# Performance work log

Hardware: AMD Instinct MI355X
Metric: run time of the kernel (lower is better)

Reference implementation:

```python
import jax, jax.numpy as jnp
import numpy as np

NUM_CLASS = 31
B = 4096
F_IN = 2048
F_BOT = 256


def setup_inputs() -> dict:
    key = jax.random.key(0)
    ks = jax.random.split(key, 6)
    return {
        "source": jax.random.normal(ks[0], (B, F_IN), dtype=jnp.float32),
        "target": jax.random.normal(ks[1], (B, F_IN), dtype=jnp.float32),
        "W_b": jax.random.normal(ks[2], (F_IN, F_BOT), dtype=jnp.float32) * (1.0 / np.sqrt(F_IN)),
        "b_b": jnp.zeros((F_BOT,), dtype=jnp.float32),
        "W_c": jax.random.normal(ks[3], (F_BOT, NUM_CLASS), dtype=jnp.float32) * (1.0 / np.sqrt(F_BOT)),
        "b_c": jnp.zeros((NUM_CLASS,), dtype=jnp.float32),
        "source_label": jax.random.randint(ks[4], (B,), 0, NUM_CLASS, dtype=jnp.int64),
    }


def _conf_margin(logits, labels):
    # get_confidence_output_margin: softmax confidence margin vs best wrong class
    conf = jax.nn.softmax(logits, axis=-1)
    mask = jax.nn.one_hot(labels, NUM_CLASS, dtype=conf.dtype)
    targets_conf = jnp.sum(conf * mask, axis=1)
    max_excl_conf = jnp.max(conf * (1.0 - mask), axis=1)
    return targets_conf - max_excl_conf


def _pairwise_sqdist(s, t):
    # ||x_p - x_q||^2 computed as a single GEMM + broadcast (replaces python double loop)
    s2 = jnp.sum(s * s, axis=1)  # [Bs]
    t2 = jnp.sum(t * t, axis=1)  # [Bt]
    d2 = s2[:, None] + t2[None, :] - 2.0 * (s @ t.T)
    return jnp.maximum(d2, 0.0)


def reference(source, target, W_b, b_b, W_c, b_c, source_label):
    # bottleneck: Linear + ReLU (shared weights for both domains)
    src = jax.nn.relu(source @ W_b + b_b)  # [B, 256]
    tar = jax.nn.relu(target @ W_b + b_b)  # [B, 256]

    src_clf = src @ W_c + b_c  # [B, 31]
    tar_clf = tar @ W_c + b_c  # [B, 31]

    # cross entropy on source
    logp = jax.nn.log_softmax(src_clf, axis=-1)
    clf_loss = -jnp.mean(jnp.take_along_axis(logp, source_label[:, None], axis=1))

    src_margin = _conf_margin(src_clf, source_label)
    tar_margin = _conf_margin(tar_clf, jnp.argmax(tar_clf, axis=1))

    # no_grad diagnostics: MMD + Gaussian kernel means (amplitude=1, sigma in {1,5})
    delta = jnp.mean(src, axis=0) - jnp.mean(tar, axis=0)
    curr_mmd = jax.lax.stop_gradient(delta @ delta)
    d2 = _pairwise_sqdist(src, tar)  # [B, B]
    curr_gk1 = jax.lax.stop_gradient(jnp.mean(jnp.exp(-0.5 * d2)))
    curr_gk5 = jax.lax.stop_gradient(jnp.mean(jnp.exp(-d2 / 50.0)))

    return jnp.concatenate([
        jnp.stack([clf_loss, curr_mmd, curr_gk1, curr_gk5]),
        src_margin,
        tar_margin,
    ])  # [4 + 2B]
```

## Files before the change

kernel.cpp:

```cpp
#include <hip/hip_runtime.h>
#include <stdint.h>

#define DI __device__ __forceinline__

typedef float f32x4 __attribute__((ext_vector_type(4)));
typedef short bf16x8 __attribute__((ext_vector_type(8)));

DI uint16_t f2bf(float f) {
    union { float f; uint32_t u; } v; v.f = f;
    uint32_t r = v.u + 0x7FFF + ((v.u >> 16) & 1);
    return (uint16_t)(r >> 16);
}
DI float bf2f(uint16_t h) {
    union { uint32_t u; float f; } v; v.u = ((uint32_t)h) << 16;
    return v.f;
}
DI void gl_lds16(const void* g, void* l) {
    __builtin_amdgcn_global_load_lds(
        (__attribute__((address_space(1))) void*)(uintptr_t)g,
        (__attribute__((address_space(3))) void*)(uintptr_t)l,
        16, 0, 0);
}

__global__ void k_init(const float* __restrict__ Wc, uint16_t* __restrict__ WcT,
                       float* __restrict__ accs) {
    int tid = threadIdx.x;
    if (tid < 4) accs[tid] = 0.f;
    for (int idx = tid; idx < 32 * 256; idx += 256) {
        int n = idx >> 8, k = idx & 255;
        WcT[idx] = (n < 31) ? f2bf(Wc[k * 31 + n]) : (uint16_t)0;
    }
}

__global__ void k_transpose_wb(const float* __restrict__ Wb, uint16_t* __restrict__ WbT) {
    __shared__ float t[32][33];
    int kb = blockIdx.x, nb = blockIdx.y;
    int tx = threadIdx.x & 31, ty0 = (threadIdx.x >> 5) * 4;
    for (int i = 0; i < 4; ++i)
        t[ty0 + i][tx] = Wb[(kb * 32 + ty0 + i) * 256 + nb * 32 + tx];
    __syncthreads();
    for (int i = 0; i < 4; ++i)
        WbT[(nb * 32 + ty0 + i) * 2048 + kb * 32 + tx] = f2bf(t[tx][ty0 + i]);
}

__launch_bounds__(256)
__global__ void k_bottleneck(const float* __restrict__ src, const float* __restrict__ tgt,
                             const uint16_t* __restrict__ WbT, const float* __restrict__ bb,
                             uint16_t* __restrict__ Y) {
    __shared__ __align__(16) uint8_t lds[20480];
    int tid = threadIdx.x;
    int lane = tid & 63, w = tid >> 6;
    int bm = blockIdx.x >> 1, bn = blockIdx.x & 1;
    int m0 = bm * 32;
    const float* X = (m0 < 4096) ? (src + (size_t)m0 * 2048)
                                 : (tgt + (size_t)(m0 - 4096) * 2048);
    int ar = tid >> 3, akb = (tid >> 2) & 1, ap = tid & 3;
    int ac = ap ^ (ar & 3) ^ ((ar >> 2) & 3);
    const float* Ag = X + ar * 2048 + akb * 32 + ac * 8;
    uint8_t* Aw = lds + akb * 2048 + ar * 64 + ap * 16;
    int cc = (lane >> 4) ^ (lane & 3) ^ ((lane >> 2) & 3);
    f32x4 acc[2][2] = {};
    for (int t = 0; t < 32; ++t) {
        int k0 = t * 64;
        if (t) __syncthreads();
        for (int i = 0; i < 4; ++i) {
            int s = w * 4 + i;
            int kb = s >> 3, r0 = (s & 7) * 16;
            int r = r0 + (lane >> 2), p = lane & 3;
            int c = p ^ (r & 3) ^ ((r >> 2) & 3);
            gl_lds16(WbT + (size_t)(bn * 128 + r) * 2048 + k0 + kb * 32 + c * 8,
                     lds + 4096 + s * 1024);
        }
        float4 x0 = *(const float4*)(Ag + k0);
        float4 x1 = *(const float4*)(Ag + k0 + 4);
        uint4 u;
        u.x = (uint32_t)f2bf(x0.x) | ((uint32_t)f2bf(x0.y) << 16);
        u.y = (uint32_t)f2bf(x0.z) | ((uint32_t)f2bf(x0.w) << 16);
        u.z = (uint32_t)f2bf(x1.x) | ((uint32_t)f2bf(x1.y) << 16);
        u.w = (uint32_t)f2bf(x1.z) | ((uint32_t)f2bf(x1.w) << 16);
        *(uint4*)Aw = u;
        __syncthreads();
        for (int kb = 0; kb < 2; ++kb) {
            bf16x8 a[2], b[2];
            for (int mi = 0; mi < 2; ++mi) {
                int r = mi * 16 + (lane & 15);
                a[mi] = *(const bf16x8*)(lds + kb * 2048 + r * 64 + cc * 16);
            }
            for (int nf = 0; nf < 2; ++nf) {
                int rn = w * 32 + nf * 16 + (lane & 15);
                b[nf] = *(const bf16x8*)(lds + 4096 + kb * 8192 + rn * 64 + cc * 16);
            }
            for (int mi = 0; mi < 2; ++mi)
                for (int nf = 0; nf < 2; ++nf)
                    acc[mi][nf] = __builtin_amdgcn_mfma_f32_16x16x32_bf16(
                        a[mi], b[nf], acc[mi][nf], 0, 0, 0);
        }
    }
    for (int mi = 0; mi < 2; ++mi)
        for (int nf = 0; nf < 2; ++nf) {
            int col = bn * 128 + w * 32 + nf * 16 + (lane & 15);
            float bias = bb[col];
            for (int j = 0; j < 4; ++j) {
                int row = m0 + mi * 16 + (lane >> 4) * 4 + j;
                float v = acc[mi][nf][j] + bias;
                v = fmaxf(v, 0.f);
                Y[(size_t)row * 256 + col] = f2bf(v);
            }
        }
}

__launch_bounds__(256)
__global__ void k_stats(const uint16_t* __restrict__ Y, float* __restrict__ s2t2,
                        float* __restrict__ colsum_part) {
    __shared__ float cs[4][256];
    int tid = threadIdx.x, lane = tid & 63, w = tid >> 6;
    int r0 = blockIdx.x * 32 + w * 8;
    float c0 = 0.f, c1 = 0.f, c2 = 0.f, c3 = 0.f;
    for (int i = 0; i < 8; ++i) {
        int row = r0 + i;
        ushort4 v = *(const ushort4*)(Y + (size_t)row * 256 + lane * 4);
        float a = bf2f(v.x), b = bf2f(v.y), c = bf2f(v.z), d = bf2f(v.w);
        c0 += a; c1 += b; c2 += c; c3 += d;
        float s = a * a + b * b + c * c + d * d;
        for (int m = 1; m < 64; m <<= 1) s += __shfl_xor(s, m);
        if (lane == 0) s2t2[row] = s;
    }
    cs[w][lane * 4 + 0] = c0;
    cs[w][lane * 4 + 1] = c1;
    cs[w][lane * 4 + 2] = c2;
    cs[w][lane * 4 + 3] = c3;
    __syncthreads();
    colsum_part[blockIdx.x * 256 + tid] =
        cs[0][tid] + cs[1][tid] + cs[2][tid] + cs[3][tid];
}

__launch_bounds__(256)
__global__ void k_classifier(const uint16_t* __restrict__ Y, const uint16_t* __restrict__ WcT,
                             const float* __restrict__ bc, const int* __restrict__ labels,
                             float* __restrict__ out_margin, float* __restrict__ ce_acc) {
    __shared__ __align__(16) uint8_t lds[49152];
    int tid = threadIdx.x, lane = tid & 63, w = tid >> 6;
    int m0 = blockIdx.x * 64;
    int cc = (lane >> 4) ^ (lane & 3) ^ ((lane >> 2) & 3);
    for (int s = w; s < 48; s += 4) {
        int r, p, c;
        if (s < 32) {
            int kb = s >> 2, r0 = (s & 3) * 16;
            r = r0 + (lane >> 2); p = lane & 3;
            c = p ^ (r & 3) ^ ((r >> 2) & 3);
            gl_lds16(Y + (size_t)(m0 + r) * 256 + kb * 32 + c * 8, lds + s * 1024);
        } else {
            int s2 = s - 32;
            int kb = s2 >> 1, r0 = (s2 & 1) * 16;
            r = r0 + (lane >> 2); p = lane & 3;
            c = p ^ (r & 3) ^ ((r >> 2) & 3);
            gl_lds16(WcT + r * 256 + kb * 32 + c * 8, lds + 32768 + s2 * 1024);
        }
    }
    __syncthreads();
    f32x4 acc[2] = {};
    for (int kb = 0; kb < 8; ++kb) {
        int r = w * 16 + (lane & 15);
        bf16x8 a = *(const bf16x8*)(lds + kb * 4096 + r * 64 + cc * 16);
        for (int nf = 0; nf < 2; ++nf) {
            int rn = nf * 16 + (lane & 15);
            bf16x8 b = *(const bf16x8*)(lds + 32768 + kb * 2048 + rn * 64 + cc * 16);
            acc[nf] = __builtin_amdgcn_mfma_f32_16x16x32_bf16(a, b, acc[nf], 0, 0, 0);
        }
    }
    int c0 = lane & 15, c1 = 16 + c0;
    float bc0 = bc[c0];
    float bc1 = (c1 < 31) ? bc[c1] : 0.f;
    bool is_src = (m0 < 4096);
    float ce_local = 0.f;
    for (int j = 0; j < 4; ++j) {
        int row = m0 + w * 16 + (lane >> 4) * 4 + j;
        float v0 = acc[0][j] + bc0;
        float v1 = (c1 < 31) ? (acc[1][j] + bc1) : -1e30f;
        float mx = fmaxf(v0, v1);
        for (int m = 1; m < 16; m <<= 1) mx = fmaxf(mx, __shfl_xor(mx, m, 16));
        float e0 = __expf(v0 - mx);
        float e1 = (c1 < 31) ? __expf(v1 - mx) : 0.f;
        float ssum = e0 + e1;
        for (int m = 1; m < 16; m <<= 1) ssum += __shfl_xor(ssum, m, 16);
        float inv = 1.f / ssum;
        float conf0 = e0 * inv, conf1 = e1 * inv;
        int lab;
        if (is_src) {
            lab = labels[row];
        } else {
            float bv; int bi;
            if (v0 >= v1) { bv = v0; bi = c0; } else { bv = v1; bi = c1; }
            for (int m = 1; m < 16; m <<= 1) {
                float ov = __shfl_xor(bv, m, 16);
                int oi = __shfl_xor(bi, m, 16);
                if (ov > bv || (ov == bv && oi < bi)) { bv = ov; bi = oi; }
            }
            lab = bi;
        }
        float tc = (c0 == lab ? conf0 : 0.f) + (c1 == lab ? conf1 : 0.f);
        for (int m = 1; m < 16; m <<= 1) tc += __shfl_xor(tc, m, 16);
        float ex = fmaxf(c0 == lab ? -1.f : conf0,
                         (c1 == lab || c1 >= 31) ? -1.f : conf1);
        for (int m = 1; m < 16; m <<= 1) ex = fmaxf(ex, __shfl_xor(ex, m, 16));
        if (c0 == 0) out_margin[row] = tc - ex;
        if (is_src) {
            float vl = (c0 == lab) ? v0 : ((c1 == lab) ? v1 : -1e30f);
            for (int m = 1; m < 16; m <<= 1) vl = fmaxf(vl, __shfl_xor(vl, m, 16));
            if (c0 == 0) ce_local += -(vl - mx - __logf(ssum));
        }
    }
    if (is_src) {
        ce_local += __shfl_xor(ce_local, 16);
        ce_local += __shfl_xor(ce_local, 32);
        if (lane == 0) atomicAdd(ce_acc, ce_local);
    }
}

__launch_bounds__(256)
__global__ void k_pairwise(const uint16_t* __restrict__ Y, const float* __restrict__ s2t2,
                           float* __restrict__ gk_part) {
    __shared__ __align__(16) uint8_t lds[65536];
    int tid = threadIdx.x, lane = tid & 63, w = tid >> 6;
    int m0 = blockIdx.x * 128, n0 = blockIdx.y * 128;
    int cc = (lane >> 4) ^ (lane & 3) ^ ((lane >> 2) & 3);
    int wm = (w & 1) * 64, wn = (w >> 1) * 64;
    f32x4 acc[4][4] = {};
    for (int h = 0; h < 2; ++h) {
        if (h) __syncthreads();
        int k0 = h * 128;
        for (int i = 0; i < 8; ++i) {
            int s = w * 8 + i;
            int kb = s >> 3, r0 = (s & 7) * 16;
            int r = r0 + (lane >> 2), p = lane & 3;
            int c = p ^ (r & 3) ^ ((r >> 2) & 3);
            gl_lds16(Y + (size_t)(m0 + r) * 256 + k0 + kb * 32 + c * 8, lds + s * 1024);
            gl_lds16(Y + (size_t)(4096 + n0 + r) * 256 + k0 + kb * 32 + c * 8,
                     lds + 32768 + s * 1024);
        }
        __syncthreads();
        for (int kb = 0; kb < 4; ++kb) {
            bf16x8 a[4], b[4];
            for (int mi = 0; mi < 4; ++mi) {
                int r = wm + mi * 16 + (lane & 15);
                a[mi] = *(const bf16x8*)(lds + kb * 8192 + r * 64 + cc * 16);
            }
            for (int nf = 0; nf < 4; ++nf) {
                int rn = wn + nf * 16 + (lane & 15);
                b[nf] = *(const bf16x8*)(lds + 32768 + kb * 8192 + rn * 64 + cc * 16);
            }
            for (int mi = 0; mi < 4; ++mi)
                for (int nf = 0; nf < 4; ++nf)
                    acc[mi][nf] = __builtin_amdgcn_mfma_f32_16x16x32_bf16(
                        a[mi], b[nf], acc[mi][nf], 0, 0, 0);
        }
    }
    float t2v[4];
    for (int nf = 0; nf < 4; ++nf)
        t2v[nf] = s2t2[4096 + n0 + wn + nf * 16 + (lane & 15)];
    float g1 = 0.f, g5 = 0.f;
    for (int mi = 0; mi < 4; ++mi) {
        int rbase = m0 + wm + mi * 16 + (lane >> 4) * 4;
        float s2v[4];
        for (int j = 0; j < 4; ++j) s2v[j] = s2t2[rbase + j];
        for (int nf = 0; nf < 4; ++nf)
            for (int j = 0; j < 4; ++j) {
                float d2 = s2v[j] + t2v[nf] - 2.f * acc[mi][nf][j];
                d2 = fmaxf(d2, 0.f);
                g1 += __expf(-0.5f * d2);
                g5 += __expf(-0.02f * d2);
            }
    }
    for (int m = 1; m < 64; m <<= 1) { g1 += __shfl_xor(g1, m); g5 += __shfl_xor(g5, m); }
    __syncthreads();
    float* red = (float*)lds;
    if (lane == 0) { red[w * 2] = g1; red[w * 2 + 1] = g5; }
    __syncthreads();
    if (tid == 0) {
        int bid = blockIdx.y * 32 + blockIdx.x;
        gk_part[bid * 2]     = red[0] + red[2] + red[4] + red[6];
        gk_part[bid * 2 + 1] = red[1] + red[3] + red[5] + red[7];
    }
}

__global__ void k_finalize(const float* __restrict__ colsum_part,
                           const float* __restrict__ gk_part,
                           const float* __restrict__ accs, float* __restrict__ d_out) {
    __shared__ float red[12];
    int tid = threadIdx.x, lane = tid & 63, w = tid >> 6;
    float cs = 0.f, ct = 0.f;
    for (int b = 0; b < 128; ++b)   cs += colsum_part[b * 256 + tid];
    for (int b = 128; b < 256; ++b) ct += colsum_part[b * 256 + tid];
    float delta = (cs - ct) * (1.f / 4096.f);
    float sq = delta * delta;
    float g1 = 0.f, g5 = 0.f;
    for (int i = 0; i < 4; ++i) {
        int p = tid * 4 + i;
        g1 += gk_part[p * 2];
        g5 += gk_part[p * 2 + 1];
    }
    for (int m = 1; m < 64; m <<= 1) {
        sq += __shfl_xor(sq, m);
        g1 += __shfl_xor(g1, m);
        g5 += __shfl_xor(g5, m);
    }
    if (lane == 0) { red[w * 3] = sq; red[w * 3 + 1] = g1; red[w * 3 + 2] = g5; }
    __syncthreads();
    if (tid == 0) {
        d_out[0] = accs[0] * (1.f / 4096.f);
        d_out[1] = red[0] + red[3] + red[6] + red[9];
        d_out[2] = (red[1] + red[4] + red[7] + red[10]) * 5.9604644775390625e-08f;
        d_out[3] = (red[2] + red[5] + red[8] + red[11]) * 5.9604644775390625e-08f;
    }
}

extern "C" void kernel_launch(void* const* d_in, const int* in_sizes, int n_in,
                              void* d_out, int out_size, void* d_ws, size_t ws_size,
                              hipStream_t stream) {
    const float* source = (const float*)d_in[0];
    const float* target = (const float*)d_in[1];
    const float* Wb     = (const float*)d_in[2];
    const float* bb     = (const float*)d_in[3];
    const float* Wc     = (const float*)d_in[4];
    const float* bc     = (const float*)d_in[5];
    const int*   labels = (const int*)d_in[6];
    float* out = (float*)d_out;
    uint8_t* ws = (uint8_t*)d_ws;

    uint16_t* Y    = (uint16_t*)(ws);
    uint16_t* WbT  = (uint16_t*)(ws + 4194304);
    uint16_t* WcT  = (uint16_t*)(ws + 5242880);
    float*    s2t2 = (float*)(ws + 5259264);
    float*    accs = (float*)(ws + 5292032);
    float*    colsum_part = (float*)(ws + 4194304);
    float*    gk_part     = (float*)(ws + 4194304 + 262144);

    k_init<<<1, 256, 0, stream>>>(Wc, WcT, accs);
    k_transpose_wb<<<dim3(64, 8), 256, 0, stream>>>(Wb, WbT);
    k_bottleneck<<<512, 256, 0, stream>>>(source, target, WbT, bb, Y);
    k_stats<<<256, 256, 0, stream>>>(Y, s2t2, colsum_part);
    k_classifier<<<128, 256, 0, stream>>>(Y, WcT, bc, labels, out + 4, accs);
    k_pairwise<<<dim3(32, 32), 256, 0, stream>>>(Y, s2t2, gk_part);
    k_finalize<<<1, 256, 0, stream>>>(colsum_part, gk_part, accs, out);
}
```

Measured before the change: 180.1 us.

## Double-buffer bottleneck GEMM LDS and prefetch next A/B tiles

Doubles the LDS allocation so the bottleneck GEMM keeps two stages of A and B tiles. The next tile's B is loaded into LDS and the next A rows are prefetched into registers while MFMAs run on the current stage. Explicit vmcnt/lgkmcnt waits plus a single barrier per stage replace the two syncthreads per iteration, which is meant to hide global memory latency behind compute. In exchange, the larger LDS footprint may lower occupancy, and the hand-written waitcnt counts are fragile.

```diff
diff --git a/kernel.cpp b/kernel.cpp
--- a/kernel.cpp
+++ b/kernel.cpp
@@ -47,7 +47,7 @@
 __global__ void k_bottleneck(const float* __restrict__ src, const float* __restrict__ tgt,
                              const uint16_t* __restrict__ WbT, const float* __restrict__ bb,
                              uint16_t* __restrict__ Y) {
-    __shared__ __align__(16) uint8_t lds[20480];
+    __shared__ __align__(16) uint8_t lds[40960];
     int tid = threadIdx.x;
     int lane = tid & 63, w = tid >> 6;
     int bm = blockIdx.x >> 1, bn = blockIdx.x & 1;
@@ -57,45 +57,117 @@
     int ar = tid >> 3, akb = (tid >> 2) & 1, ap = tid & 3;
     int ac = ap ^ (ar & 3) ^ ((ar >> 2) & 3);
     const float* Ag = X + ar * 2048 + akb * 32 + ac * 8;
-    uint8_t* Aw = lds + akb * 2048 + ar * 64 + ap * 16;
+    const int AwOff = akb * 2048 + ar * 64 + ap * 16;
     int cc = (lane >> 4) ^ (lane & 3) ^ ((lane >> 2) & 3);
+    const uint16_t* Bg0; const uint16_t* Bg1; const uint16_t* Bg2; const uint16_t* Bg3;
+    {
+        int p = lane & 3;
+        int i0 = w * 4;
+        #define BGADDR(ii) ({ int s_ = i0 + (ii); int kb_ = s_ >> 3; \
+            int r_ = (s_ & 7) * 16 + (lane >> 2); \
+            int c_ = p ^ (r_ & 3) ^ ((r_ >> 2) & 3); \
+            WbT + (size_t)(bn * 128 + r_) * 2048 + kb_ * 32 + c_ * 8; })
+        Bg0 = BGADDR(0); Bg1 = BGADDR(1); Bg2 = BGADDR(2); Bg3 = BGADDR(3);
+        #undef BGADDR
+    }
+    const int lbB = 8192 + w * 4096;
+
     f32x4 acc[2][2] = {};
-    for (int t = 0; t < 32; ++t) {
-        int k0 = t * 64;
-        if (t) __syncthreads();
-        for (int i = 0; i < 4; ++i) {
-            int s = w * 4 + i;
-            int kb = s >> 3, r0 = (s & 7) * 16;
-            int r = r0 + (lane >> 2), p = lane & 3;
-            int c = p ^ (r & 3) ^ ((r >> 2) & 3);
-            gl_lds16(WbT + (size_t)(bn * 128 + r) * 2048 + k0 + kb * 32 + c * 8,
-                     lds + 4096 + s * 1024);
-        }
-        float4 x0 = *(const float4*)(Ag + k0);
-        float4 x1 = *(const float4*)(Ag + k0 + 4);
-        uint4 u;
-        u.x = (uint32_t)f2bf(x0.x) | ((uint32_t)f2bf(x0.y) << 16);
-        u.y = (uint32_t)f2bf(x0.z) | ((uint32_t)f2bf(x0.w) << 16);
-        u.z = (uint32_t)f2bf(x1.x) | ((uint32_t)f2bf(x1.y) << 16);
-        u.w = (uint32_t)f2bf(x1.z) | ((uint32_t)f2bf(x1.w) << 16);
-        *(uint4*)Aw = u;
-        __syncthreads();
-        for (int kb = 0; kb < 2; ++kb) {
-            bf16x8 a[2], b[2];
-            for (int mi = 0; mi < 2; ++mi) {
-                int r = mi * 16 + (lane & 15);
-                a[mi] = *(const bf16x8*)(lds + kb * 2048 + r * 64 + cc * 16);
-            }
-            for (int nf = 0; nf < 2; ++nf) {
-                int rn = w * 32 + nf * 16 + (lane & 15);
-                b[nf] = *(const bf16x8*)(lds + 4096 + kb * 8192 + rn * 64 + cc * 16);
-            }
-            for (int mi = 0; mi < 2; ++mi)
-                for (int nf = 0; nf < 2; ++nf)
-                    acc[mi][nf] = __builtin_amdgcn_mfma_f32_16x16x32_bf16(
-                        a[mi], b[nf], acc[mi][nf], 0, 0, 0);
-        }
-    }
+    float4 rE0, rE1, rO0, rO1;
+
+    #define STAGE_B(par, k0) do { \
+        gl_lds16(Bg0 + (k0), lds + lbB + (par) * 16384 + 0);    \
+        gl_lds16(Bg1 + (k0), lds + lbB + (par) * 16384 + 1024); \
+        gl_lds16(Bg2 + (k0), lds + lbB + (par) * 16384 + 2048); \
+        gl_lds16(Bg3 + (k0), lds + lbB + (par) * 16384 + 3072); \
+    } while (0)
+
+    #define WRITE_A(par, r0v, r1v) do { \
+        uint4 u_; \
+        u_.x = (uint32_t)f2bf((r0v).x) | ((uint32_t)f2bf((r0v).y) << 16); \
+        u_.y = (uint32_t)f2bf((r0v).z) | ((uint32_t)f2bf((r0v).w) << 16); \
+        u_.z = (uint32_t)f2bf((r1v).x) | ((uint32_t)f2bf((r1v).y) << 16); \
+        u_.w = (uint32_t)f2bf((r1v).z) | ((uint32_t)f2bf((r1v).w) << 16); \
+        *(uint4*)(lds + (par) * 4096 + AwOff) = u_; \
+    } while (0)
+
+    #define COMPUTE(par) do { \
+        _Pragma("unroll") \
+        for (int kb = 0; kb < 2; ++kb) { \
+            bf16x8 a_[2], b_[2]; \
+            _Pragma("unroll") \
+            for (int mi = 0; mi < 2; ++mi) \
+                a_[mi] = *(const bf16x8*)(lds + (par) * 4096 + kb * 2048 + \
+                                          (mi * 16 + (lane & 15)) * 64 + cc * 16); \
+            _Pragma("unroll") \
+            for (int nf = 0; nf < 2; ++nf) \
+                b_[nf] = *(const bf16x8*)(lds + 8192 + (par) * 16384 + kb * 8192 + \
+                                          (w * 32 + nf * 16 + (lane & 15)) * 64 + cc * 16); \
+            _Pragma("unroll") \
+            for (int mi = 0; mi < 2; ++mi) \
+                _Pragma("unroll") \
+                for (int nf = 0; nf < 2; ++nf) \
+                    acc[mi][nf] = __builtin_amdgcn_mfma_f32_16x16x32_bf16( \
+                        a_[mi], b_[nf], acc[mi][nf], 0, 0, 0); \
+        } \
+    } while (0)
+
+    #define FENCE() asm volatile("" ::: "memory")
+
+    STAGE_B(0, 0);
+    FENCE();
+    rE0 = *(const float4*)(Ag);
+    rE1 = *(const float4*)(Ag + 4);
+    FENCE();
+    rO0 = *(const float4*)(Ag + 64);
+    rO1 = *(const float4*)(Ag + 68);
+    asm volatile("s_waitcnt vmcnt(2)" ::: "memory");
+    WRITE_A(0, rE0, rE1);
+    asm volatile("s_waitcnt lgkmcnt(0)" ::: "memory");
+    __builtin_amdgcn_s_barrier();
+
+    for (int tt = 0; tt < 15; ++tt) {
+        {
+            int t = 2 * tt;
+            STAGE_B(1, (t + 1) * 64);
+            FENCE();
+            rE0 = *(const float4*)(Ag + (t + 2) * 64);
+            rE1 = *(const float4*)(Ag + (t + 2) * 64 + 4);
+            FENCE();
+            COMPUTE(0);
+            asm volatile("s_waitcnt vmcnt(6)" ::: "memory");
+            WRITE_A(1, rO0, rO1);
+            asm volatile("s_waitcnt vmcnt(2) lgkmcnt(0)" ::: "memory");
+            __builtin_amdgcn_s_barrier();
+        }
+        {
+            int t = 2 * tt + 1;
+            STAGE_B(0, (t + 1) * 64);
+            FENCE();
+            rO0 = *(const float4*)(Ag + (t + 2) * 64);
+            rO1 = *(const float4*)(Ag + (t + 2) * 64 + 4);
+            FENCE();
+            COMPUTE(1);
+            asm volatile("s_waitcnt vmcnt(6)" ::: "memory");
+            WRITE_A(0, rE0, rE1);
+            asm volatile("s_waitcnt vmcnt(2) lgkmcnt(0)" ::: "memory");
+            __builtin_amdgcn_s_barrier();
+        }
+    }
+    STAGE_B(1, 31 * 64);
+    FENCE();
+    COMPUTE(0);
+    asm volatile("s_waitcnt vmcnt(4)" ::: "memory");
+    WRITE_A(1, rO0, rO1);
+    asm volatile("s_waitcnt vmcnt(0) lgkmcnt(0)" ::: "memory");
+    __builtin_amdgcn_s_barrier();
+    COMPUTE(1);
+
+    #undef STAGE_B
+    #undef WRITE_A
+    #undef COMPUTE
+    #undef FENCE
+
     for (int mi = 0; mi < 2; ++mi)
         for (int nf = 0; nf < 2; ++nf) {
             int col = bn * 128 + w * 32 + nf * 16 + (lane & 15);
```

New measurement: 174.6 us. -3.0%, faster.

## Restructure bottleneck GEMM as split-K across waves with LDS reduction

Applied to the files above, without the earlier changes.

The bottleneck GEMM now runs 256 blocks of 512 threads. Each block covers 32 rows and all 256 output columns, so every source/target row is read from global memory once instead of twice. Each of 8 waves handles a 256-wide K slice, loading A fragments directly from global into registers with double buffering and B fragments directly from global without LDS staging. Partial results are then reduced across waves through a 64KB LDS buffer before the bias and ReLU are applied. This removes the per-iteration syncthreads and the LDS staging, at the cost of 128 accumulator registers per thread, uncoalesced direct global B loads, and a reduction epilogue.

```diff
diff --git a/kernel.cpp b/kernel.cpp
--- a/kernel.cpp
+++ b/kernel.cpp
@@ -14,6 +14,14 @@
 DI float bf2f(uint16_t h) {
     union { uint32_t u; float f; } v; v.u = ((uint32_t)h) << 16;
     return v.f;
+}
+DI bf16x8 cvt8(float4 lo, float4 hi) {
+    union { uint4 u; bf16x8 v; } x;
+    x.u.x = (uint32_t)f2bf(lo.x) | ((uint32_t)f2bf(lo.y) << 16);
+    x.u.y = (uint32_t)f2bf(lo.z) | ((uint32_t)f2bf(lo.w) << 16);
+    x.u.z = (uint32_t)f2bf(hi.x) | ((uint32_t)f2bf(hi.y) << 16);
+    x.u.w = (uint32_t)f2bf(hi.z) | ((uint32_t)f2bf(hi.w) << 16);
+    return x.v;
 }
 DI void gl_lds16(const void* g, void* l) {
     __builtin_amdgcn_global_load_lds(
@@ -43,70 +51,83 @@
         WbT[(nb * 32 + ty0 + i) * 2048 + kb * 32 + tx] = f2bf(t[tx][ty0 + i]);
 }
 
-__launch_bounds__(256)
+__launch_bounds__(512, 2)
 __global__ void k_bottleneck(const float* __restrict__ src, const float* __restrict__ tgt,
                              const uint16_t* __restrict__ WbT, const float* __restrict__ bb,
                              uint16_t* __restrict__ Y) {
-    __shared__ __align__(16) uint8_t lds[20480];
-    int tid = threadIdx.x;
-    int lane = tid & 63, w = tid >> 6;
-    int bm = blockIdx.x >> 1, bn = blockIdx.x & 1;
-    int m0 = bm * 32;
+    __shared__ float red[8][2048];
+    int tid = threadIdx.x, lane = tid & 63, w = tid >> 6;
+    int m0 = blockIdx.x * 32;
     const float* X = (m0 < 4096) ? (src + (size_t)m0 * 2048)
                                  : (tgt + (size_t)(m0 - 4096) * 2048);
-    int ar = tid >> 3, akb = (tid >> 2) & 1, ap = tid & 3;
-    int ac = ap ^ (ar & 3) ^ ((ar >> 2) & 3);
-    const float* Ag = X + ar * 2048 + akb * 32 + ac * 8;
-    uint8_t* Aw = lds + akb * 2048 + ar * 64 + ap * 16;
-    int cc = (lane >> 4) ^ (lane & 3) ^ ((lane >> 2) & 3);
-    f32x4 acc[2][2] = {};
-    for (int t = 0; t < 32; ++t) {
-        int k0 = t * 64;
-        if (t) __syncthreads();
-        for (int i = 0; i < 4; ++i) {
-            int s = w * 4 + i;
-            int kb = s >> 3, r0 = (s & 7) * 16;
-            int r = r0 + (lane >> 2), p = lane & 3;
-            int c = p ^ (r & 3) ^ ((r >> 2) & 3);
-            gl_lds16(WbT + (size_t)(bn * 128 + r) * 2048 + k0 + kb * 32 + c * 8,
-                     lds + 4096 + s * 1024);
-        }
-        float4 x0 = *(const float4*)(Ag + k0);
-        float4 x1 = *(const float4*)(Ag + k0 + 4);
-        uint4 u;
-        u.x = (uint32_t)f2bf(x0.x) | ((uint32_t)f2bf(x0.y) << 16);
-        u.y = (uint32_t)f2bf(x0.z) | ((uint32_t)f2bf(x0.w) << 16);
-        u.z = (uint32_t)f2bf(x1.x) | ((uint32_t)f2bf(x1.y) << 16);
-        u.w = (uint32_t)f2bf(x1.z) | ((uint32_t)f2bf(x1.w) << 16);
-        *(uint4*)Aw = u;
-        __syncthreads();
-        for (int kb = 0; kb < 2; ++kb) {
-            bf16x8 a[2], b[2];
+    int fr = lane & 15;
+    int kq = lane >> 4;
+    const float* Ag = X + (size_t)fr * 2048 + w * 256 + kq * 8;
+    const uint16_t* Bg = WbT + (size_t)fr * 2048 + w * 256 + kq * 8;
+
+    f32x4 acc[2][16] = {};
+
+    float4 aA[2][2][2];
+    #pragma unroll
+    for (int mi = 0; mi < 2; ++mi) {
+        aA[0][mi][0] = *(const float4*)(Ag + mi * 32768);
+        aA[0][mi][1] = *(const float4*)(Ag + mi * 32768 + 4);
+        aA[1][mi][0] = *(const float4*)(Ag + mi * 32768 + 32);
+        aA[1][mi][1] = *(const float4*)(Ag + mi * 32768 + 36);
+    }
+    #pragma unroll
+    for (int t = 0; t < 8; ++t) {
+        bf16x8 af[2];
+        #pragma unroll
+        for (int mi = 0; mi < 2; ++mi)
+            af[mi] = cvt8(aA[t & 1][mi][0], aA[t & 1][mi][1]);
+        if (t < 6) {
+            #pragma unroll
             for (int mi = 0; mi < 2; ++mi) {
-                int r = mi * 16 + (lane & 15);
-                a[mi] = *(const bf16x8*)(lds + kb * 2048 + r * 64 + cc * 16);
-            }
-            for (int nf = 0; nf < 2; ++nf) {
-                int rn = w * 32 + nf * 16 + (lane & 15);
-                b[nf] = *(const bf16x8*)(lds + 4096 + kb * 8192 + rn * 64 + cc * 16);
-            }
-            for (int mi = 0; mi < 2; ++mi)
-                for (int nf = 0; nf < 2; ++nf)
-                    acc[mi][nf] = __builtin_amdgcn_mfma_f32_16x16x32_bf16(
-                        a[mi], b[nf], acc[mi][nf], 0, 0, 0);
-        }
-    }
-    for (int mi = 0; mi < 2; ++mi)
-        for (int nf = 0; nf < 2; ++nf) {
-            int col = bn * 128 + w * 32 + nf * 16 + (lane & 15);
-            float bias = bb[col];
-            for (int j = 0; j < 4; ++j) {
-                int row = m0 + mi * 16 + (lane >> 4) * 4 + j;
-                float v = acc[mi][nf][j] + bias;
-                v = fmaxf(v, 0.f);
-                Y[(size_t)row * 256 + col] = f2bf(v);
-            }
-        }
+                aA[t & 1][mi][0] = *(const float4*)(Ag + mi * 32768 + (t + 2) * 32);
+                aA[t & 1][mi][1] = *(const float4*)(Ag + mi * 32768 + (t + 2) * 32 + 4);
+            }
+        }
+        #pragma unroll
+        for (int nf = 0; nf < 16; ++nf) {
+            bf16x8 bv = *(const bf16x8*)(Bg + (size_t)nf * 32768 + t * 32);
+            acc[0][nf] = __builtin_amdgcn_mfma_f32_16x16x32_bf16(af[0], bv, acc[0][nf], 0, 0, 0);
+            acc[1][nf] = __builtin_amdgcn_mfma_f32_16x16x32_bf16(af[1], bv, acc[1][nf], 0, 0, 0);
+        }
+    }
+
+    int e0 = tid * 4;
+    int rl = e0 >> 8;
+    int col = e0 & 255;
+    float4 bias = *(const float4*)(bb + col);
+    #pragma unroll
+    for (int mi = 0; mi < 2; ++mi) {
+        #pragma unroll
+        for (int half = 0; half < 2; ++half) {
+            if (mi || half) __syncthreads();
+            if ((kq >> 1) == half) {
+                #pragma unroll
+                for (int nf = 0; nf < 16; ++nf)
+                    #pragma unroll
+                    for (int j = 0; j < 4; ++j)
+                        red[w][((kq & 1) * 4 + j) * 256 + nf * 16 + fr] = acc[mi][nf][j];
+            }
+            __syncthreads();
+            float4 s = {0.f, 0.f, 0.f, 0.f};
+            #pragma unroll
+            for (int p = 0; p < 8; ++p) {
+                float4 v = *(const float4*)(&red[p][e0]);
+                s.x += v.x; s.y += v.y; s.z += v.z; s.w += v.w;
+            }
+            int row = m0 + mi * 16 + half * 8 + rl;
+            ushort4 o;
+            o.x = f2bf(fmaxf(s.x + bias.x, 0.f));
+            o.y = f2bf(fmaxf(s.y + bias.y, 0.f));
+            o.z = f2bf(fmaxf(s.z + bias.z, 0.f));
+            o.w = f2bf(fmaxf(s.w + bias.w, 0.f));
+            *(ushort4*)(Y + (size_t)row * 256 + col) = o;
+        }
+    }
 }
 
 __launch_bounds__(256)
@@ -337,7 +358,7 @@
 
     k_init<<<1, 256, 0, stream>>>(Wc, WcT, accs);
     k_transpose_wb<<<dim3(64, 8), 256, 0, stream>>>(Wb, WbT);
-    k_bottleneck<<<512, 256, 0, stream>>>(source, target, WbT, bb, Y);
+    k_bottleneck<<<256, 512, 0, stream>>>(source, target, WbT, bb, Y);
     k_stats<<<256, 256, 0, stream>>>(Y, s2t2, colsum_part);
     k_classifier<<<128, 256, 0, stream>>>(Y, WcT, bc, labels, out + 4, accs);
     k_pairwise<<<dim3(32, 32), 256, 0, stream>>>(Y, s2t2, gk_part);
```

Measured after the change: 190.9 us. 6.0% more time.
